# Optimization experiments

Measured on AMD Instinct MI355X. Metric: run time of the kernel, lower is better.

Reference implementation:

```python
import jax, jax.numpy as jnp
import numpy as np

N_NODES = 50000
N_EDGES = 1500000
FEAT = 128
CUTOFF = 5.0


def setup_inputs() -> dict:
    key = jax.random.key(0)
    k_x, k_ei, k_el, k_w = jax.random.split(key, 4)
    x = jax.random.normal(k_x, (N_NODES, FEAT), dtype=jnp.float32)
    edge_index = jax.random.randint(k_ei, (2, N_EDGES), 0, N_NODES, dtype=jnp.int64)
    edge_len = jax.random.uniform(k_el, (N_EDGES,), dtype=jnp.float32) * CUTOFF
    # learned params: equivariant mix (dense linear for scalar irreps, no bias),
    # log of distance scale (init sharpness=6.0), and 1->1 filter linear.
    W_mix = jax.random.normal(k_w, (FEAT, FEAT), dtype=jnp.float32) / np.sqrt(FEAT)
    log_scale = jnp.asarray(np.log(6.0), dtype=jnp.float32)
    filter_w = jnp.asarray(0.7, dtype=jnp.float32)
    filter_b = jnp.asarray(0.1, dtype=jnp.float32)
    return {"x": x, "edge_index": edge_index, "edge_len": edge_len,
            "W_mix": W_mix, "log_scale": log_scale,
            "filter_w": filter_w, "filter_b": filter_b}


def reference(x, edge_index, edge_len, W_mix, log_scale, filter_w, filter_b):
    sender = edge_index[0]
    receiver = edge_index[1]
    n_nodes = x.shape[0]

    scale = jnp.exp(log_scale).astype(edge_len.dtype)
    decay = jnp.exp(-jnp.maximum(edge_len / (scale + 1e-6), 0.0) ** 2)  # [E]
    gate = jax.nn.sigmoid(edge_len * filter_w + filter_b)               # [E]
    weights = jnp.nan_to_num(decay * gate, nan=0.0, posinf=0.0, neginf=0.0)

    # gather-scale-scatter: messages [E, F] -> per-node sum
    messages = weights[:, None].astype(x.dtype) * x[sender]
    agg = jax.ops.segment_sum(messages, receiver, num_segments=n_nodes)
    degree = jax.ops.segment_sum(jnp.ones_like(edge_len), receiver,
                                 num_segments=n_nodes)
    agg = agg / jnp.maximum(degree, 1.0)[:, None].astype(x.dtype)

    return x + agg @ W_mix
```

## Files before the change

kernel.cpp:

```cpp
#include <hip/hip_runtime.h>
#include <math.h>

#define FEAT 128
#define BSHIFT 6
#define BNODES 64
#define FB 16
#define CAP_REC 1024
#define NBUCK_MAX 1024
#define EPB 4096

__device__ __forceinline__ float edge_weight(float d, float scale, float fw, float fb) {
    float t = fmaxf(d / scale, 0.0f);
    float decay = expf(-t * t);
    float g = 1.0f / (1.0f + expf(-(d * fw + fb)));
    float w = decay * g;
    if (!isfinite(w)) w = 0.0f;
    return w;
}

__device__ __forceinline__ unsigned int bf16_rne(float f) {
    unsigned int b = __float_as_uint(f);
    return (b + 0x7FFFu + ((b >> 16) & 1u)) >> 16;
}

__device__ __forceinline__ void accum8(float acc[8], uint4 u, float w) {
    acc[0] = fmaf(w, __uint_as_float(u.x << 16), acc[0]);
    acc[1] = fmaf(w, __uint_as_float(u.x & 0xFFFF0000u), acc[1]);
    acc[2] = fmaf(w, __uint_as_float(u.y << 16), acc[2]);
    acc[3] = fmaf(w, __uint_as_float(u.y & 0xFFFF0000u), acc[3]);
    acc[4] = fmaf(w, __uint_as_float(u.z << 16), acc[4]);
    acc[5] = fmaf(w, __uint_as_float(u.z & 0xFFFF0000u), acc[5]);
    acc[6] = fmaf(w, __uint_as_float(u.w << 16), acc[6]);
    acc[7] = fmaf(w, __uint_as_float(u.w & 0xFFFF0000u), acc[7]);
}

__global__ __launch_bounds__(256) void convert_scatter_kernel(
    const float4* __restrict__ x4, uint2* __restrict__ xbf, int n4,
    const int* __restrict__ sender, const int* __restrict__ recv,
    const float* __restrict__ edge_len,
    const float* __restrict__ log_scale, const float* __restrict__ filter_w,
    const float* __restrict__ filter_b,
    int* __restrict__ gcnt, unsigned long long* __restrict__ buf,
    int E, int nbuck, int cap, int nchunk) {
    __shared__ int cnt[NBUCK_MAX];
    const int tid = threadIdx.x;

    if ((int)blockIdx.x >= nchunk) {
        int i = ((int)blockIdx.x - nchunk) * 256 + tid;
        if (i >= n4) return;
        float4 v = x4[i];
        uint2 o;
        o.x = (bf16_rne(v.y) << 16) | bf16_rne(v.x);
        o.y = (bf16_rne(v.w) << 16) | bf16_rne(v.z);
        xbf[i] = o;
        return;
    }

    const int c = blockIdx.x;
    for (int i = tid; i < nbuck; i += 256) cnt[i] = 0;
    __syncthreads();
    const int base = c * EPB;
    const int end = min(base + EPB, E);
    for (int e = base + tid; e < end; e += 256)
        atomicAdd(&cnt[recv[e] >> BSHIFT], 1);
    __syncthreads();
    for (int i = tid; i < nbuck; i += 256) {
        int cc = cnt[i];
        int b0 = cc ? atomicAdd(&gcnt[i], cc) : 0;
        cnt[i] = i * cap + b0;
    }
    __syncthreads();
    float scale = expf(log_scale[0]) + 1e-6f;
    float fw = filter_w[0], fb = filter_b[0];
    for (int e = base + tid; e < end; e += 256) {
        int r = recv[e];
        int s = sender[e];
        float w = edge_weight(edge_len[e], scale, fw, fb);
        int bk = r >> BSHIFT;
        int pos = atomicAdd(&cnt[bk], 1);
        if (pos < (bk + 1) * cap)
            buf[pos] = ((unsigned long long)__float_as_uint(w) << 32)
                     | (unsigned int)(s & 0xFFFF)
                     | ((unsigned int)(r & (BNODES - 1)) << 16);
    }
}

__global__ __launch_bounds__(256) void bucket_sort_aggregate_kernel(
    const uint4* __restrict__ xbf4, const unsigned long long* __restrict__ buf,
    const int* __restrict__ gcnt, uint4* __restrict__ agg_bf4,
    int* __restrict__ deg, int N, int cap) {
    __shared__ unsigned long long recS[CAP_REC];
    __shared__ int cnt16[FB];
    __shared__ int segoff[FB + 1];

    int cb = blockIdx.x >> 2;
    int q  = blockIdx.x & 3;
    int n0 = (cb << BSHIFT) + (q << 4);
    int nEnd = min(n0 + FB, N);
    int lo = cb * cap;
    int hi = lo + min(gcnt[cb], cap);
    int tid = threadIdx.x;
    int lane = tid & 15;
    int grp = tid >> 4;

    float acc[8] = {0.f,0.f,0.f,0.f,0.f,0.f,0.f,0.f};
    int dcnt = 0;

    for (int pos = lo; pos < hi; pos += CAP_REC) {
        int cnt = min(CAP_REC, hi - pos);
        if (tid < FB) cnt16[tid] = 0;
        __syncthreads();

        unsigned long long rec[CAP_REC / 256];
        int lr[CAP_REC / 256];
#pragma unroll
        for (int k = 0; k < CAP_REC / 256; ++k) {
            int i = k * 256 + tid;
            lr[k] = -1;
            if (i < cnt) {
                unsigned long long r = buf[pos + i];
                int l6 = ((unsigned int)r >> 16) & 63;
                if ((l6 >> 4) == q) {
                    int l = l6 & 15;
                    int rk = atomicAdd(&cnt16[l], 1);
                    lr[k] = (rk << 4) | l;
                    rec[k] = r;
                }
            }
        }
        __syncthreads();
        if (tid == 0) {
            int run = 0;
#pragma unroll
            for (int l = 0; l < FB; ++l) { segoff[l] = run; run += cnt16[l]; }
            segoff[FB] = run;
        }
        __syncthreads();
#pragma unroll
        for (int k = 0; k < CAP_REC / 256; ++k)
            if (lr[k] >= 0) recS[segoff[lr[k] & 15] + (lr[k] >> 4)] = rec[k];
        __syncthreads();

        {
            int s0 = segoff[grp], s1 = segoff[grp + 1];
            dcnt += s1 - s0;
            int i = s0;
            for (; i + 4 <= s1; i += 4) {
                unsigned long long r0 = recS[i];
                unsigned long long r1 = recS[i + 1];
                unsigned long long r2 = recS[i + 2];
                unsigned long long r3 = recS[i + 3];
                float w0 = __uint_as_float((unsigned int)(r0 >> 32));
                float w1 = __uint_as_float((unsigned int)(r1 >> 32));
                float w2 = __uint_as_float((unsigned int)(r2 >> 32));
                float w3 = __uint_as_float((unsigned int)(r3 >> 32));
                int s0i = (unsigned int)r0 & 0xFFFF;
                int s1i = (unsigned int)r1 & 0xFFFF;
                int s2i = (unsigned int)r2 & 0xFFFF;
                int s3i = (unsigned int)r3 & 0xFFFF;
                uint4 u0 = xbf4[(size_t)s0i * 16 + lane];
                uint4 u1 = xbf4[(size_t)s1i * 16 + lane];
                uint4 u2 = xbf4[(size_t)s2i * 16 + lane];
                uint4 u3 = xbf4[(size_t)s3i * 16 + lane];
                accum8(acc, u0, w0);
                accum8(acc, u1, w1);
                accum8(acc, u2, w2);
                accum8(acc, u3, w3);
            }
            for (; i < s1; ++i) {
                unsigned long long ra = recS[i];
                float wa = __uint_as_float((unsigned int)(ra >> 32));
                int sa = (unsigned int)ra & 0xFFFF;
                uint4 ua = xbf4[(size_t)sa * 16 + lane];
                accum8(acc, ua, wa);
            }
        }
        __syncthreads();
    }

    {
        int n = n0 + grp;
        if (n < nEnd) {
            uint4 o;
            o.x = (bf16_rne(acc[1]) << 16) | bf16_rne(acc[0]);
            o.y = (bf16_rne(acc[3]) << 16) | bf16_rne(acc[2]);
            o.z = (bf16_rne(acc[5]) << 16) | bf16_rne(acc[4]);
            o.w = (bf16_rne(acc[7]) << 16) | bf16_rne(acc[6]);
            agg_bf4[(size_t)n * 16 + lane] = o;
            if (lane == 0) deg[n] = dcnt;
        }
    }
}

__global__ __launch_bounds__(256) void finalize_kernel(
    const float* __restrict__ x, const uint4* __restrict__ agg_bf4,
    const int* __restrict__ deg, const float* __restrict__ Wm,
    float* __restrict__ out, int N) {
    __shared__ float aggS[64 * 128];
    __shared__ float Ws[128 * 64];
    const int n0 = blockIdx.x * 64;

    for (int i = threadIdx.x; i < 64 * 16; i += 256) {
        int r = i >> 4;
        int q = i & 15;
        int n = n0 + r;
        uint4 u = make_uint4(0u, 0u, 0u, 0u);
        if (n < N) u = agg_bf4[(size_t)n * 16 + q];
        float4 f0, f1;
        f0.x = __uint_as_float(u.x << 16);
        f0.y = __uint_as_float(u.x & 0xFFFF0000u);
        f0.z = __uint_as_float(u.y << 16);
        f0.w = __uint_as_float(u.y & 0xFFFF0000u);
        f1.x = __uint_as_float(u.z << 16);
        f1.y = __uint_as_float(u.z & 0xFFFF0000u);
        f1.z = __uint_as_float(u.w << 16);
        f1.w = __uint_as_float(u.w & 0xFFFF0000u);
        int m = (r >> 2) & 7;
        ((float4*)aggS)[r * 32 + ((2 * q) ^ m)] = f0;
        ((float4*)aggS)[r * 32 + ((2 * q + 1) ^ m)] = f1;
    }

    const int tc = threadIdx.x & 15;
    const int tr = threadIdx.x >> 4;

    float invd[4];
#pragma unroll
    for (int i = 0; i < 4; ++i) {
        int n = n0 + 4 * tr + i;
        float degf = 1.0f;
        if (n < N) degf = fmaxf((float)deg[n], 1.0f);
        invd[i] = 1.0f / degf;
    }

    for (int h = 0; h < 2; ++h) {
        for (int i = threadIdx.x; i < 128 * 16; i += 256) {
            int k = i >> 4;
            int j4 = i & 15;
            ((float4*)Ws)[k * 16 + j4] = ((const float4*)Wm)[k * 32 + h * 16 + j4];
        }
        __syncthreads();

        float acc[4][4];
#pragma unroll
        for (int i = 0; i < 4; ++i)
#pragma unroll
            for (int c = 0; c < 4; ++c) acc[i][c] = 0.f;

#pragma unroll 4
        for (int k0 = 0; k0 < 128; k0 += 4) {
            float4 ar4[4];
            const int chunk = (k0 >> 2) ^ (tr & 7);
#pragma unroll
            for (int i = 0; i < 4; ++i) {
                int r = 4 * tr + i;
                ar4[i] = ((const float4*)aggS)[r * 32 + chunk];
            }
            float4 wv4[4];
#pragma unroll
            for (int kk = 0; kk < 4; ++kk)
                wv4[kk] = *(const float4*)&Ws[(k0 + kk) * 64 + tc * 4];

            float wvv[4][4];
#pragma unroll
            for (int kk = 0; kk < 4; ++kk) {
                wvv[kk][0] = wv4[kk].x; wvv[kk][1] = wv4[kk].y;
                wvv[kk][2] = wv4[kk].z; wvv[kk][3] = wv4[kk].w;
            }
#pragma unroll
            for (int i = 0; i < 4; ++i) {
                float av[4] = {ar4[i].x, ar4[i].y, ar4[i].z, ar4[i].w};
#pragma unroll
                for (int kk = 0; kk < 4; ++kk)
#pragma unroll
                    for (int c = 0; c < 4; ++c)
                        acc[i][c] = fmaf(av[kk], wvv[kk][c], acc[i][c]);
            }
        }

#pragma unroll
        for (int i = 0; i < 4; ++i) {
            int n = n0 + 4 * tr + i;
            if (n < N) {
                size_t base = (size_t)n * FEAT + h * 64 + tc * 4;
                float4 xv = *(const float4*)&x[base];
                float4 o;
                o.x = xv.x + invd[i] * acc[i][0];
                o.y = xv.y + invd[i] * acc[i][1];
                o.z = xv.z + invd[i] * acc[i][2];
                o.w = xv.w + invd[i] * acc[i][3];
                *(float4*)&out[base] = o;
            }
        }
        __syncthreads();
    }
}

__global__ __launch_bounds__(256) void scatter_fallback(
    const float4* __restrict__ x4, const int* __restrict__ sender,
    const int* __restrict__ receiver, const float* __restrict__ edge_len,
    const float* __restrict__ log_scale, const float* __restrict__ filter_w,
    const float* __restrict__ filter_b, float* __restrict__ agg,
    float* __restrict__ deg, int E) {
    int gid = blockIdx.x * 256 + threadIdx.x;
    int e = gid >> 5;
    if (e >= E) return;
    int lane = gid & 31;
    int s = sender[e];
    int r = receiver[e];
    float scale = expf(log_scale[0]) + 1e-6f;
    float w = edge_weight(edge_len[e], scale, filter_w[0], filter_b[0]);
    float4 xv = x4[s * (FEAT / 4) + lane];
    float* dst = agg + (size_t)r * FEAT + lane * 4;
    unsafeAtomicAdd(dst + 0, w * xv.x);
    unsafeAtomicAdd(dst + 1, w * xv.y);
    unsafeAtomicAdd(dst + 2, w * xv.z);
    unsafeAtomicAdd(dst + 3, w * xv.w);
    if (lane == 0) unsafeAtomicAdd(&deg[r], 1.0f);
}

__global__ __launch_bounds__(256) void finalize_fallback(
    const float* __restrict__ x, const float* __restrict__ agg,
    const float* __restrict__ deg, const float* __restrict__ Wm,
    float* __restrict__ out, int N) {
    __shared__ float Wsf[FEAT * FEAT];
    for (int i = threadIdx.x * 4; i < FEAT * FEAT; i += 256 * 4)
        *(float4*)&Wsf[i] = *(const float4*)&Wm[i];
    __syncthreads();
    int half = threadIdx.x >> 7;
    int j = threadIdx.x & (FEAT - 1);
    for (int n0 = blockIdx.x * 2; n0 < N; n0 += gridDim.x * 2) {
        int n = n0 + half;
        if (n < N) {
            const float* arow = agg + (size_t)n * FEAT;
            float acc = 0.0f;
#pragma unroll 16
            for (int k = 0; k < FEAT; ++k) acc = fmaf(arow[k], Wsf[k * FEAT + j], acc);
            float invd = 1.0f / fmaxf(deg[n], 1.0f);
            size_t idx = (size_t)n * FEAT + j;
            out[idx] = x[idx] + invd * acc;
        }
    }
}

extern "C" void kernel_launch(void* const* d_in, const int* in_sizes, int n_in,
                              void* d_out, int out_size, void* d_ws, size_t ws_size,
                              hipStream_t stream) {
    const float* x         = (const float*)d_in[0];
    const int*   ei        = (const int*)d_in[1];
    const float* edge_len  = (const float*)d_in[2];
    const float* W_mix     = (const float*)d_in[3];
    const float* log_scale = (const float*)d_in[4];
    const float* filter_w  = (const float*)d_in[5];
    const float* filter_b  = (const float*)d_in[6];
    float* out = (float*)d_out;

    const int N = in_sizes[0] / FEAT;
    const int E = in_sizes[1] / 2;
    const int* sender   = ei;
    const int* receiver = ei + E;
    const int nbuck = (N + BNODES - 1) >> BSHIFT;
    const int nchunk = (E + EPB - 1) / EPB;

    size_t xbf_bytes  = (size_t)N * FEAT * 2;
    size_t aggb_bytes = (size_t)N * FEAT * 2;
    size_t gcnt_bytes = (((size_t)nbuck * 4) + 63) & ~(size_t)63;
    size_t deg_bytes  = (((size_t)N * 4) + 63) & ~(size_t)63;

    int mean = E / nbuck + 1;
    size_t head = xbf_bytes + aggb_bytes + gcnt_bytes + deg_bytes;
    size_t avail = (ws_size > head) ? ws_size - head : 0;
    int cap = (2 * mean + 512 + 63) & ~63;
    int capmax = (int)((avail / ((size_t)nbuck * 8)) & ~(size_t)63);
    if (cap > capmax) cap = capmax;
    int sigma5 = 5 * (int)sqrtf((float)mean) + 64;
    bool ok = (N <= 65536) && (nbuck <= NBUCK_MAX) && (cap >= mean + sigma5);

    if (ok) {
        char* p = (char*)d_ws;
        uint2* xbf    = (uint2*)p;                        p += xbf_bytes;
        uint4* agg_bf = (uint4*)p;                        p += aggb_bytes;
        int* gcnt     = (int*)p;                          p += gcnt_bytes;
        int* deg      = (int*)p;                          p += deg_bytes;
        unsigned long long* buf = (unsigned long long*)p;

        (void)hipMemsetAsync(gcnt, 0, (size_t)nbuck * sizeof(int), stream);

        int n4 = N * (FEAT / 4);
        int cblocks = (n4 + 255) / 256;
        convert_scatter_kernel<<<nchunk + cblocks, 256, 0, stream>>>(
            (const float4*)x, xbf, n4, sender, receiver, edge_len,
            log_scale, filter_w, filter_b, gcnt, buf, E, nbuck, cap, nchunk);
        bucket_sort_aggregate_kernel<<<nbuck * 4, 256, 0, stream>>>(
            (const uint4*)xbf, buf, gcnt, agg_bf, deg, N, cap);
        int fblocks = (N + 63) / 64;
        finalize_kernel<<<fblocks, 256, 0, stream>>>(
            x, (const uint4*)agg_bf, deg, W_mix, out, N);
    } else {
        float* agg = (float*)d_ws;
        float* degf = agg + (size_t)N * FEAT;
        (void)hipMemsetAsync(agg, 0, ((size_t)N * FEAT + N) * sizeof(float), stream);
        int sblocks = (E * 32 + 255) / 256;
        scatter_fallback<<<sblocks, 256, 0, stream>>>(
            (const float4*)x, sender, receiver, edge_len,
            log_scale, filter_w, filter_b, agg, degf, E);
        finalize_fallback<<<512, 256, 0, stream>>>(x, agg, degf, W_mix, out, N);
    }
}
```

Measured before the change: 227.3 us.

## Locally sort edge records per chunk and aggregate one bucket per block

The scatter kernel now counting-sorts each chunk's edge records by bucket in shared memory with a block-wide prefix scan, then writes them out contiguously per bucket, so global writes are coalesced instead of scattered one by one. The aggregate kernel drops the four-way split of each 64-node bucket, so one 512-thread block reads the bucket once and each thread group handles two nodes. This removes the fourfold rereading and filtering of bucket records. In exchange it adds shared memory (a 32KB record buffer plus several bucket arrays), extra barriers for the scan, and fewer, larger aggregate blocks, which may reduce occupancy.

```diff
diff --git a/kernel.cpp b/kernel.cpp
--- a/kernel.cpp
+++ b/kernel.cpp
@@ -4,8 +4,7 @@
 #define FEAT 128
 #define BSHIFT 6
 #define BNODES 64
-#define FB 16
-#define CAP_REC 1024
+#define CAP2 2048
 #define NBUCK_MAX 1024
 #define EPB 4096
 
@@ -42,7 +41,12 @@
     const float* __restrict__ filter_b,
     int* __restrict__ gcnt, unsigned long long* __restrict__ buf,
     int E, int nbuck, int cap, int nchunk) {
+    __shared__ unsigned long long recS[EPB];
     __shared__ int cnt[NBUCK_MAX];
+    __shared__ int segoff[NBUCK_MAX];
+    __shared__ int segcur[NBUCK_MAX];
+    __shared__ int resbase[NBUCK_MAX];
+    __shared__ int part[256];
     const int tid = threadIdx.x;
 
     if ((int)blockIdx.x >= nchunk) {
@@ -61,15 +65,45 @@
     __syncthreads();
     const int base = c * EPB;
     const int end = min(base + EPB, E);
+    const int cntE = end - base;
     for (int e = base + tid; e < end; e += 256)
         atomicAdd(&cnt[recv[e] >> BSHIFT], 1);
     __syncthreads();
+
+    {
+        int i0 = tid * 4;
+        int v0 = 0, v1 = 0, v2 = 0, v3 = 0;
+        if (i0 < nbuck) {
+            v0 = cnt[i0];
+            v1 = (i0 + 1 < nbuck) ? cnt[i0 + 1] : 0;
+            v2 = (i0 + 2 < nbuck) ? cnt[i0 + 2] : 0;
+            v3 = (i0 + 3 < nbuck) ? cnt[i0 + 3] : 0;
+        }
+        int s = v0 + v1 + v2 + v3;
+        part[tid] = s;
+        __syncthreads();
+        for (int d = 1; d < 256; d <<= 1) {
+            int t = (tid >= d) ? part[tid - d] : 0;
+            __syncthreads();
+            part[tid] += t;
+            __syncthreads();
+        }
+        int run = part[tid] - s;
+        if (i0 < nbuck) {
+            segoff[i0] = run; run += v0;
+            if (i0 + 1 < nbuck) { segoff[i0 + 1] = run; run += v1; }
+            if (i0 + 2 < nbuck) { segoff[i0 + 2] = run; run += v2; }
+            if (i0 + 3 < nbuck) { segoff[i0 + 3] = run; run += v3; }
+        }
+    }
     for (int i = tid; i < nbuck; i += 256) {
         int cc = cnt[i];
         int b0 = cc ? atomicAdd(&gcnt[i], cc) : 0;
-        cnt[i] = i * cap + b0;
+        resbase[i] = i * cap + b0;
+        segcur[i] = segoff[i];
     }
     __syncthreads();
+
     float scale = expf(log_scale[0]) + 1e-6f;
     float fw = filter_w[0], fb = filter_b[0];
     for (int e = base + tid; e < end; e += 256) {
@@ -77,73 +111,81 @@
         int s = sender[e];
         float w = edge_weight(edge_len[e], scale, fw, fb);
         int bk = r >> BSHIFT;
-        int pos = atomicAdd(&cnt[bk], 1);
+        int j = atomicAdd(&segcur[bk], 1);
+        recS[j] = ((unsigned long long)__float_as_uint(w) << 32)
+                | (unsigned int)(s & 0xFFFF)
+                | ((unsigned int)(r & (BNODES - 1)) << 16)
+                | ((unsigned int)(bk & 1023) << 22);
+    }
+    __syncthreads();
+
+    for (int j = tid; j < cntE; j += 256) {
+        unsigned long long rec = recS[j];
+        int bk = ((unsigned int)rec >> 22) & 1023;
+        int pos = resbase[bk] + (j - segoff[bk]);
         if (pos < (bk + 1) * cap)
-            buf[pos] = ((unsigned long long)__float_as_uint(w) << 32)
-                     | (unsigned int)(s & 0xFFFF)
-                     | ((unsigned int)(r & (BNODES - 1)) << 16);
-    }
-}
-
-__global__ __launch_bounds__(256) void bucket_sort_aggregate_kernel(
+            buf[pos] = rec;
+    }
+}
+
+__global__ __launch_bounds__(512) void bucket_sort_aggregate_kernel(
     const uint4* __restrict__ xbf4, const unsigned long long* __restrict__ buf,
     const int* __restrict__ gcnt, uint4* __restrict__ agg_bf4,
     int* __restrict__ deg, int N, int cap) {
-    __shared__ unsigned long long recS[CAP_REC];
-    __shared__ int cnt16[FB];
-    __shared__ int segoff[FB + 1];
-
-    int cb = blockIdx.x >> 2;
-    int q  = blockIdx.x & 3;
-    int n0 = (cb << BSHIFT) + (q << 4);
-    int nEnd = min(n0 + FB, N);
-    int lo = cb * cap;
-    int hi = lo + min(gcnt[cb], cap);
-    int tid = threadIdx.x;
-    int lane = tid & 15;
-    int grp = tid >> 4;
-
-    float acc[8] = {0.f,0.f,0.f,0.f,0.f,0.f,0.f,0.f};
-    int dcnt = 0;
-
-    for (int pos = lo; pos < hi; pos += CAP_REC) {
-        int cnt = min(CAP_REC, hi - pos);
-        if (tid < FB) cnt16[tid] = 0;
-        __syncthreads();
-
-        unsigned long long rec[CAP_REC / 256];
-        int lr[CAP_REC / 256];
-#pragma unroll
-        for (int k = 0; k < CAP_REC / 256; ++k) {
-            int i = k * 256 + tid;
-            lr[k] = -1;
+    __shared__ unsigned long long recS[CAP2];
+    __shared__ int cnt64[BNODES];
+    __shared__ int segoff[BNODES + 1];
+
+    const int b = blockIdx.x;
+    const int n0 = b << BSHIFT;
+    const int tid = threadIdx.x;
+    const int lane = tid & 15;
+    const int grp = tid >> 4;
+    const int lo = b * cap;
+    const int hi = lo + min(gcnt[b], cap);
+
+    float acc[2][8] = {{0.f,0.f,0.f,0.f,0.f,0.f,0.f,0.f},
+                       {0.f,0.f,0.f,0.f,0.f,0.f,0.f,0.f}};
+    int dcnt[2] = {0, 0};
+
+    for (int pos = lo; pos < hi; pos += CAP2) {
+        int cnt = min(CAP2, hi - pos);
+        if (tid < BNODES) cnt64[tid] = 0;
+        __syncthreads();
+
+        unsigned long long rec[CAP2 / 512];
+        int rnk[CAP2 / 512];
+        int locl[CAP2 / 512];
+#pragma unroll
+        for (int k = 0; k < CAP2 / 512; ++k) {
+            int i = k * 512 + tid;
+            rnk[k] = -1;
             if (i < cnt) {
                 unsigned long long r = buf[pos + i];
-                int l6 = ((unsigned int)r >> 16) & 63;
-                if ((l6 >> 4) == q) {
-                    int l = l6 & 15;
-                    int rk = atomicAdd(&cnt16[l], 1);
-                    lr[k] = (rk << 4) | l;
-                    rec[k] = r;
-                }
+                int l = ((unsigned int)r >> 16) & (BNODES - 1);
+                rec[k] = r;
+                locl[k] = l;
+                rnk[k] = atomicAdd(&cnt64[l], 1);
             }
         }
         __syncthreads();
         if (tid == 0) {
             int run = 0;
 #pragma unroll
-            for (int l = 0; l < FB; ++l) { segoff[l] = run; run += cnt16[l]; }
-            segoff[FB] = run;
-        }
-        __syncthreads();
-#pragma unroll
-        for (int k = 0; k < CAP_REC / 256; ++k)
-            if (lr[k] >= 0) recS[segoff[lr[k] & 15] + (lr[k] >> 4)] = rec[k];
-        __syncthreads();
-
-        {
-            int s0 = segoff[grp], s1 = segoff[grp + 1];
-            dcnt += s1 - s0;
+            for (int l = 0; l < BNODES; ++l) { segoff[l] = run; run += cnt64[l]; }
+            segoff[BNODES] = run;
+        }
+        __syncthreads();
+#pragma unroll
+        for (int k = 0; k < CAP2 / 512; ++k)
+            if (rnk[k] >= 0) recS[segoff[locl[k]] + rnk[k]] = rec[k];
+        __syncthreads();
+
+#pragma unroll
+        for (int which = 0; which < 2; ++which) {
+            int l = grp + which * 32;
+            int s0 = segoff[l], s1 = segoff[l + 1];
+            dcnt[which] += s1 - s0;
             int i = s0;
             for (; i + 4 <= s1; i += 4) {
                 unsigned long long r0 = recS[i];
@@ -162,32 +204,33 @@
                 uint4 u1 = xbf4[(size_t)s1i * 16 + lane];
                 uint4 u2 = xbf4[(size_t)s2i * 16 + lane];
                 uint4 u3 = xbf4[(size_t)s3i * 16 + lane];
-                accum8(acc, u0, w0);
-                accum8(acc, u1, w1);
-                accum8(acc, u2, w2);
-                accum8(acc, u3, w3);
+                accum8(acc[which], u0, w0);
+                accum8(acc[which], u1, w1);
+                accum8(acc[which], u2, w2);
+                accum8(acc[which], u3, w3);
             }
             for (; i < s1; ++i) {
                 unsigned long long ra = recS[i];
                 float wa = __uint_as_float((unsigned int)(ra >> 32));
                 int sa = (unsigned int)ra & 0xFFFF;
                 uint4 ua = xbf4[(size_t)sa * 16 + lane];
-                accum8(acc, ua, wa);
-            }
-        }
-        __syncthreads();
-    }
-
-    {
-        int n = n0 + grp;
-        if (n < nEnd) {
+                accum8(acc[which], ua, wa);
+            }
+        }
+        __syncthreads();
+    }
+
+#pragma unroll
+    for (int which = 0; which < 2; ++which) {
+        int n = n0 + grp + which * 32;
+        if (n < N) {
             uint4 o;
-            o.x = (bf16_rne(acc[1]) << 16) | bf16_rne(acc[0]);
-            o.y = (bf16_rne(acc[3]) << 16) | bf16_rne(acc[2]);
-            o.z = (bf16_rne(acc[5]) << 16) | bf16_rne(acc[4]);
-            o.w = (bf16_rne(acc[7]) << 16) | bf16_rne(acc[6]);
+            o.x = (bf16_rne(acc[which][1]) << 16) | bf16_rne(acc[which][0]);
+            o.y = (bf16_rne(acc[which][3]) << 16) | bf16_rne(acc[which][2]);
+            o.z = (bf16_rne(acc[which][5]) << 16) | bf16_rne(acc[which][4]);
+            o.w = (bf16_rne(acc[which][7]) << 16) | bf16_rne(acc[which][6]);
             agg_bf4[(size_t)n * 16 + lane] = o;
-            if (lane == 0) deg[n] = dcnt;
+            if (lane == 0) deg[n] = dcnt[which];
         }
     }
 }
@@ -390,7 +433,7 @@
         convert_scatter_kernel<<<nchunk + cblocks, 256, 0, stream>>>(
             (const float4*)x, xbf, n4, sender, receiver, edge_len,
             log_scale, filter_w, filter_b, gcnt, buf, E, nbuck, cap, nchunk);
-        bucket_sort_aggregate_kernel<<<nbuck * 4, 256, 0, stream>>>(
+        bucket_sort_aggregate_kernel<<<nbuck, 512, 0, stream>>>(
             (const uint4*)xbf, buf, gcnt, agg_bf, deg, N, cap);
         int fblocks = (N + 63) / 64;
         finalize_kernel<<<fblocks, 256, 0, stream>>>(
```

Result: faster. 216.2 us (-4.9%).
